# Kernel tuning notes

Hardware: AMD Instinct MI355X
Metric: run time of the kernel (lower is better)

The kernel has to match this reference:

```python
import jax, jax.numpy as jnp
import numpy as np

B, N, C, H = 8, 1024, 1024, 16
HD = C // H
SCALE = HD ** -0.5

def setup_inputs() -> dict:
    key = jax.random.key(0)
    k1, k2, k3, k4 = jax.random.split(key, 4)
    x = jax.random.normal(k1, (B, N, C), dtype=jnp.float32)
    # torch nn.Linear weights: [out, in]
    w_qkv = jax.random.normal(k2, (3 * C, C), dtype=jnp.float32) * (C ** -0.5)
    w_proj = jax.random.normal(k3, (C, C), dtype=jnp.float32) * (C ** -0.5)
    b_proj = jax.random.normal(k4, (C,), dtype=jnp.float32) * 0.02
    return {"x": x, "w_qkv": w_qkv, "w_proj": w_proj, "b_proj": b_proj}

def reference(x, w_qkv, w_proj, b_proj):
    Bv, Nv, Cv = x.shape
    # qkv projection (no bias); torch Linear: x @ W^T
    qkv = jnp.einsum('bnc,dc->bnd', x, w_qkv)
    qkv = qkv.reshape(Bv, Nv, 3, H, HD).transpose(2, 0, 3, 1, 4)  # [3,B,H,N,hd]
    q, k, v = qkv[0], qkv[1], qkv[2]
    attn = jnp.einsum('bhnd,bhmd->bhnm', q, k) * SCALE  # [B,H,N,N]
    attn = jax.nn.softmax(attn, axis=-1)
    out = jnp.einsum('bhnm,bhmd->bhnd', attn, v)
    out = out.transpose(0, 2, 1, 3).reshape(Bv, Nv, Cv)
    out = jnp.einsum('bnc,dc->bnd', out, w_proj) + b_proj
    return out
```

## Files before the change

kernel.cpp:

```cpp
#include <hip/hip_runtime.h>


typedef __attribute__((ext_vector_type(8))) short bf16x8;
typedef __attribute__((ext_vector_type(4))) float f32x4;

__device__ __forceinline__ short f2bf(float f) {
    union { float f; unsigned u; } x;
    x.f = f;
    unsigned r = x.u + 0x7fffu + ((x.u >> 16) & 1u);
    return (short)(r >> 16);
}

__device__ __forceinline__ void load_lds16(const void* g, void* l) {
    __builtin_amdgcn_global_load_lds((const __attribute__((address_space(1))) unsigned*)g,
                                     (__attribute__((address_space(3))) unsigned*)l,
                                     16, 0, 0);
}

__global__ __launch_bounds__(256) void convert_all(const float* __restrict__ x,
                                                   const float* __restrict__ wqkv,
                                                   const float* __restrict__ wproj,
                                                   short* __restrict__ xb,
                                                   short* __restrict__ wqkvb,
                                                   short* __restrict__ wprojb) {
    int i = blockIdx.x * 256 + threadIdx.x;
    const float* src;
    short* dst;
    int j;
    if (i < 2097152)      { src = x;     dst = xb;     j = i; }
    else if (i < 2883584) { src = wqkv;  dst = wqkvb;  j = i - 2097152; }
    else                  { src = wproj; dst = wprojb; j = i - 2883584; }
    float4 v = *(const float4*)(src + j * 4);
    unsigned lo = (unsigned short)f2bf(v.x) | ((unsigned)(unsigned short)f2bf(v.y) << 16);
    unsigned hi = (unsigned short)f2bf(v.z) | ((unsigned)(unsigned short)f2bf(v.w) << 16);
    uint2 p; p.x = lo; p.y = hi;
    *(uint2*)(dst + j * 4) = p;
}

__global__ __launch_bounds__(256) void gemm_qkv(const short* __restrict__ A,
                                                const short* __restrict__ Bt,
                                                short* __restrict__ q,
                                                short* __restrict__ k,
                                                short* __restrict__ vt) {
    __shared__ alignas(16) short As[3][128][32];
    __shared__ alignas(16) short Bs[3][128][32];
    const int K = 1024;
    const int m0 = blockIdx.y * 128;
    const int n0 = blockIdx.x * 128;
    const int t = threadIdx.x;
    const int w = t >> 6, lane = t & 63, quad = lane >> 4, l16 = lane & 15;
    const int wm = (w >> 1) * 64, wn = (w & 1) * 64;
    const int srow = lane >> 2;
    const int sc8 = (lane & 3) * 8;

    const short* Abase = &A[(m0 + w * 32 + srow) * K + sc8];
    const short* Bbase = &Bt[(n0 + w * 32 + srow) * K + sc8];

    f32x4 acc[4][4];
    for (int mi = 0; mi < 4; ++mi)
        for (int ni = 0; ni < 4; ++ni)
            acc[mi][ni] = (f32x4){0.f, 0.f, 0.f, 0.f};

    #pragma unroll
    for (int p = 0; p < 2; ++p) {
        load_lds16(Abase + p * 32,          &As[p][w * 32][0]);
        load_lds16(Abase + 16 * K + p * 32, &As[p][w * 32 + 16][0]);
        load_lds16(Bbase + p * 32,          &Bs[p][w * 32][0]);
        load_lds16(Bbase + 16 * K + p * 32, &Bs[p][w * 32 + 16][0]);
    }

    #pragma unroll
    for (int it = 0; it < 32; ++it) {
        if (it == 31) asm volatile("s_waitcnt vmcnt(0) lgkmcnt(0)" ::: "memory");
        else          asm volatile("s_waitcnt vmcnt(4) lgkmcnt(0)" ::: "memory");
        asm volatile("s_barrier" ::: "memory");
        if (it < 30) {
            const int b2 = (it + 2) % 3;
            load_lds16(Abase + (it + 2) * 32,          &As[b2][w * 32][0]);
            load_lds16(Abase + 16 * K + (it + 2) * 32, &As[b2][w * 32 + 16][0]);
            load_lds16(Bbase + (it + 2) * 32,          &Bs[b2][w * 32][0]);
            load_lds16(Bbase + 16 * K + (it + 2) * 32, &Bs[b2][w * 32 + 16][0]);
        }
        const int cb = it % 3;
        bf16x8 af[4], bfr[4];
        for (int i = 0; i < 4; ++i) af[i]  = *(const bf16x8*)&As[cb][wm + i * 16 + l16][quad * 8];
        for (int i = 0; i < 4; ++i) bfr[i] = *(const bf16x8*)&Bs[cb][wn + i * 16 + l16][quad * 8];
        for (int mi = 0; mi < 4; ++mi)
            for (int ni = 0; ni < 4; ++ni)
                acc[mi][ni] = __builtin_amdgcn_mfma_f32_16x16x32_bf16(af[mi], bfr[ni], acc[mi][ni], 0, 0, 0);
    }

    const float QS = 0.125f * 1.44269504088896f;
    for (int ni = 0; ni < 4; ++ni) {
        int col = n0 + wn + ni * 16 + l16;
        int sect = col >> 10;
        int c = col & 1023;
        int h = c >> 6, d = c & 63;
        for (int mi = 0; mi < 4; ++mi) {
            for (int r = 0; r < 4; ++r) {
                int m = m0 + wm + mi * 16 + quad * 4 + r;
                int b = m >> 10, i = m & 1023;
                float v = acc[mi][ni][r];
                if (sect == 0)      q[((b * 16 + h) * 1024 + i) * 64 + d] = f2bf(v * QS);
                else if (sect == 1) k[((b * 16 + h) * 1024 + i) * 64 + d] = f2bf(v);
                else                vt[((b * 16 + h) * 64 + d) * 1024 + i] = f2bf(v);
            }
        }
    }
}

__global__ __launch_bounds__(256) void attn_kernel(const short* __restrict__ q,
                                                   const short* __restrict__ k,
                                                   const short* __restrict__ vt,
                                                   short* __restrict__ ao) {
    __shared__ alignas(16) short Ks[64][72];
    __shared__ alignas(16) short Vs[64][72];
    __shared__ alignas(16) short Ps[4][32][72];

    const int bh = blockIdx.y, qt = blockIdx.x;
    const int t = threadIdx.x, w = t >> 6, lane = t & 63, quad = lane >> 4, l16 = lane & 15;
    const short* qg = q  + (bh * 1024 + qt * 128) * 64;
    const short* kg = k  + bh * 65536;
    const short* vg = vt + bh * 65536;

    bf16x8 qf[2][2];
    for (int mi = 0; mi < 2; ++mi) {
        const short* qr = qg + (w * 32 + mi * 16 + l16) * 64;
        qf[mi][0] = *(const bf16x8*)(qr + quad * 8);
        qf[mi][1] = *(const bf16x8*)(qr + 32 + quad * 8);
    }

    const int r0 = t >> 3,          c80 = (t & 7) * 8;
    const int r1 = (t + 256) >> 3,  c81 = c80;

    float rs[2][4];
    f32x4 oacc[2][4];
    for (int mi = 0; mi < 2; ++mi)
        for (int r = 0; r < 4; ++r) rs[mi][r] = 0.f;
    for (int mi = 0; mi < 2; ++mi)
        for (int nt = 0; nt < 4; ++nt) oacc[mi][nt] = (f32x4){0.f, 0.f, 0.f, 0.f};

    {
        float4 a = *(const float4*)&kg[r0 * 64 + c80];
        float4 b = *(const float4*)&kg[r1 * 64 + c81];
        float4 c = *(const float4*)&vg[r0 * 1024 + c80];
        float4 d = *(const float4*)&vg[r1 * 1024 + c81];
        *(float4*)&Ks[r0][c80] = a;  *(float4*)&Ks[r1][c81] = b;
        *(float4*)&Vs[r0][c80] = c;  *(float4*)&Vs[r1][c81] = d;
    }

    for (int jt = 0; jt < 16; ++jt) {
        asm volatile("s_waitcnt lgkmcnt(0)" ::: "memory");
        asm volatile("s_barrier" ::: "memory");

        float4 kr0, kr1, vr0, vr1;
        if (jt < 15) {
            int jn = jt + 1;
            kr0 = *(const float4*)&kg[(jn * 64 + r0) * 64 + c80];
            kr1 = *(const float4*)&kg[(jn * 64 + r1) * 64 + c81];
            vr0 = *(const float4*)&vg[r0 * 1024 + jn * 64 + c80];
            vr1 = *(const float4*)&vg[r1 * 1024 + jn * 64 + c81];
        }

        bf16x8 kf[4][2], vf[4][2];
        for (int nt = 0; nt < 4; ++nt) {
            kf[nt][0] = *(const bf16x8*)&Ks[nt * 16 + l16][quad * 8];
            kf[nt][1] = *(const bf16x8*)&Ks[nt * 16 + l16][32 + quad * 8];
            vf[nt][0] = *(const bf16x8*)&Vs[nt * 16 + l16][quad * 8];
            vf[nt][1] = *(const bf16x8*)&Vs[nt * 16 + l16][32 + quad * 8];
        }
        asm volatile("s_waitcnt lgkmcnt(0)" ::: "memory");
        asm volatile("s_barrier" ::: "memory");
        if (jt < 15) {
            *(float4*)&Ks[r0][c80] = kr0;  *(float4*)&Ks[r1][c81] = kr1;
            *(float4*)&Vs[r0][c80] = vr0;  *(float4*)&Vs[r1][c81] = vr1;
        }

        for (int mi = 0; mi < 2; ++mi) {
            f32x4 s[4];
            for (int nt = 0; nt < 4; ++nt) {
                f32x4 a = (f32x4){0.f, 0.f, 0.f, 0.f};
                a = __builtin_amdgcn_mfma_f32_16x16x32_bf16(qf[mi][0], kf[nt][0], a, 0, 0, 0);
                a = __builtin_amdgcn_mfma_f32_16x16x32_bf16(qf[mi][1], kf[nt][1], a, 0, 0, 0);
                s[nt] = a;
            }
            for (int nt = 0; nt < 4; ++nt) {
                for (int r = 0; r < 4; ++r) {
                    float p = __builtin_amdgcn_exp2f(s[nt][r]);
                    rs[mi][r] += p;
                    Ps[w][mi * 16 + quad * 4 + r][nt * 16 + l16] = f2bf(p);
                }
            }
            asm volatile("s_waitcnt lgkmcnt(0)" ::: "memory");
            bf16x8 pa0 = *(const bf16x8*)&Ps[w][mi * 16 + l16][quad * 8];
            bf16x8 pa1 = *(const bf16x8*)&Ps[w][mi * 16 + l16][32 + quad * 8];
            for (int nt = 0; nt < 4; ++nt) {
                oacc[mi][nt] = __builtin_amdgcn_mfma_f32_16x16x32_bf16(pa0, vf[nt][0], oacc[mi][nt], 0, 0, 0);
                oacc[mi][nt] = __builtin_amdgcn_mfma_f32_16x16x32_bf16(pa1, vf[nt][1], oacc[mi][nt], 0, 0, 0);
            }
        }
    }

    for (int mi = 0; mi < 2; ++mi)
        for (int r = 0; r < 4; ++r)
            for (int msk = 1; msk < 16; msk <<= 1)
                rs[mi][r] += __shfl_xor(rs[mi][r], msk, 64);

    const int b = bh >> 4, h = bh & 15;
    for (int mi = 0; mi < 2; ++mi) {
        for (int r = 0; r < 4; ++r) {
            float inv = 1.0f / rs[mi][r];
            int i = qt * 128 + w * 32 + mi * 16 + quad * 4 + r;
            for (int nt = 0; nt < 4; ++nt) {
                int d = nt * 16 + l16;
                ao[(b * 1024 + i) * 1024 + h * 64 + d] = f2bf(oacc[mi][nt][r] * inv);
            }
        }
    }
}

__global__ __launch_bounds__(256) void gemm_proj(const short* __restrict__ A,
                                                 const short* __restrict__ Bt,
                                                 const float* __restrict__ bias,
                                                 float* __restrict__ out) {
    __shared__ alignas(16) short As[3][128][32];
    __shared__ alignas(16) short Bs[3][128][32];
    const int K = 1024;
    const int m0 = blockIdx.y * 128;
    const int n0 = blockIdx.x * 128;
    const int t = threadIdx.x;
    const int w = t >> 6, lane = t & 63, quad = lane >> 4, l16 = lane & 15;
    const int wm = (w >> 1) * 64, wn = (w & 1) * 64;
    const int srow = lane >> 2;
    const int sc8 = (lane & 3) * 8;

    const short* Abase = &A[(m0 + w * 32 + srow) * K + sc8];
    const short* Bbase = &Bt[(n0 + w * 32 + srow) * K + sc8];

    f32x4 acc[4][4];
    for (int mi = 0; mi < 4; ++mi)
        for (int ni = 0; ni < 4; ++ni)
            acc[mi][ni] = (f32x4){0.f, 0.f, 0.f, 0.f};

    #pragma unroll
    for (int p = 0; p < 2; ++p) {
        load_lds16(Abase + p * 32,          &As[p][w * 32][0]);
        load_lds16(Abase + 16 * K + p * 32, &As[p][w * 32 + 16][0]);
        load_lds16(Bbase + p * 32,          &Bs[p][w * 32][0]);
        load_lds16(Bbase + 16 * K + p * 32, &Bs[p][w * 32 + 16][0]);
    }

    #pragma unroll
    for (int it = 0; it < 32; ++it) {
        if (it == 31) asm volatile("s_waitcnt vmcnt(0) lgkmcnt(0)" ::: "memory");
        else          asm volatile("s_waitcnt vmcnt(4) lgkmcnt(0)" ::: "memory");
        asm volatile("s_barrier" ::: "memory");
        if (it < 30) {
            const int b2 = (it + 2) % 3;
            load_lds16(Abase + (it + 2) * 32,          &As[b2][w * 32][0]);
            load_lds16(Abase + 16 * K + (it + 2) * 32, &As[b2][w * 32 + 16][0]);
            load_lds16(Bbase + (it + 2) * 32,          &Bs[b2][w * 32][0]);
            load_lds16(Bbase + 16 * K + (it + 2) * 32, &Bs[b2][w * 32 + 16][0]);
        }
        const int cb = it % 3;
        bf16x8 af[4], bfr[4];
        for (int i = 0; i < 4; ++i) af[i]  = *(const bf16x8*)&As[cb][wm + i * 16 + l16][quad * 8];
        for (int i = 0; i < 4; ++i) bfr[i] = *(const bf16x8*)&Bs[cb][wn + i * 16 + l16][quad * 8];
        for (int mi = 0; mi < 4; ++mi)
            for (int ni = 0; ni < 4; ++ni)
                acc[mi][ni] = __builtin_amdgcn_mfma_f32_16x16x32_bf16(af[mi], bfr[ni], acc[mi][ni], 0, 0, 0);
    }

    for (int ni = 0; ni < 4; ++ni) {
        int col = n0 + wn + ni * 16 + l16;
        float bv = bias[col];
        for (int mi = 0; mi < 4; ++mi) {
            for (int r = 0; r < 4; ++r) {
                int m = m0 + wm + mi * 16 + quad * 4 + r;
                out[m * 1024 + col] = acc[mi][ni][r] + bv;
            }
        }
    }
}

extern "C" void kernel_launch(void* const* d_in, const int* in_sizes, int n_in,
                              void* d_out, int out_size, void* d_ws, size_t ws_size,
                              hipStream_t stream) {
    const float* x      = (const float*)d_in[0];
    const float* w_qkv  = (const float*)d_in[1];
    const float* w_proj = (const float*)d_in[2];
    const float* b_proj = (const float*)d_in[3];
    float* out = (float*)d_out;

    char* ws = (char*)d_ws;
    short* xb     = (short*)(ws);
    short* wqkvb  = (short*)(ws + 16777216);
    short* wprojb = (short*)(ws + 23068672);
    short* qb     = (short*)(ws + 25165824);
    short* kb     = (short*)(ws + 41943040);
    short* vtb    = (short*)(ws + 58720256);
    short* aob    = (short*)(ws + 75497472);

    convert_all<<<12288, 256, 0, stream>>>(x, w_qkv, w_proj, xb, wqkvb, wprojb);
    gemm_qkv<<<dim3(24, 64), 256, 0, stream>>>(xb, wqkvb, qb, kb, vtb);
    attn_kernel<<<dim3(8, 128), 256, 0, stream>>>(qb, kb, vtb, aob);
    gemm_proj<<<dim3(8, 64), 256, 0, stream>>>(aob, wprojb, b_proj, out);
}
```

Measured before the change: 280.3 us.

## Compute transposed S so P stays in registers, dropping the LDS round-trip

The attention kernel now computes S^T = K·Q^T, so each lane's MFMA output already matches the B-operand layout of a 16x16x16 bf16 MFMA. P therefore feeds the PV product straight from registers, and the per-warp P shared buffer with its writes, waits and reads is removed. The output is accumulated transposed (O^T = V^T·P^T), which makes the row-sum reduction shorter and lets the final store write 4 bf16 at a time. In exchange it uses twice as many smaller 16x16x16 MFMAs for PV and reads V from LDS in narrower 8-byte fragments.

```diff
diff --git a/kernel.cpp b/kernel.cpp
--- a/kernel.cpp
+++ b/kernel.cpp
@@ -2,6 +2,7 @@
 
 
 typedef __attribute__((ext_vector_type(8))) short bf16x8;
+typedef __attribute__((ext_vector_type(4))) short bf16x4;
 typedef __attribute__((ext_vector_type(4))) float f32x4;
 
 __device__ __forceinline__ short f2bf(float f) {
@@ -115,7 +116,6 @@
                                                    short* __restrict__ ao) {
     __shared__ alignas(16) short Ks[64][72];
     __shared__ alignas(16) short Vs[64][72];
-    __shared__ alignas(16) short Ps[4][32][72];
 
     const int bh = blockIdx.y, qt = blockIdx.x;
     const int t = threadIdx.x, w = t >> 6, lane = t & 63, quad = lane >> 4, l16 = lane & 15;
@@ -133,12 +133,10 @@
     const int r0 = t >> 3,          c80 = (t & 7) * 8;
     const int r1 = (t + 256) >> 3,  c81 = c80;
 
-    float rs[2][4];
-    f32x4 oacc[2][4];
+    float rs[2] = {0.f, 0.f};
+    f32x4 oaccT[2][4];
     for (int mi = 0; mi < 2; ++mi)
-        for (int r = 0; r < 4; ++r) rs[mi][r] = 0.f;
-    for (int mi = 0; mi < 2; ++mi)
-        for (int nt = 0; nt < 4; ++nt) oacc[mi][nt] = (f32x4){0.f, 0.f, 0.f, 0.f};
+        for (int dt = 0; dt < 4; ++dt) oaccT[mi][dt] = (f32x4){0.f, 0.f, 0.f, 0.f};
 
     {
         float4 a = *(const float4*)&kg[r0 * 64 + c80];
@@ -162,12 +160,13 @@
             vr1 = *(const float4*)&vg[r1 * 1024 + jn * 64 + c81];
         }
 
-        bf16x8 kf[4][2], vf[4][2];
-        for (int nt = 0; nt < 4; ++nt) {
-            kf[nt][0] = *(const bf16x8*)&Ks[nt * 16 + l16][quad * 8];
-            kf[nt][1] = *(const bf16x8*)&Ks[nt * 16 + l16][32 + quad * 8];
-            vf[nt][0] = *(const bf16x8*)&Vs[nt * 16 + l16][quad * 8];
-            vf[nt][1] = *(const bf16x8*)&Vs[nt * 16 + l16][32 + quad * 8];
+        bf16x8 kf[4][2];
+        bf16x4 vtf[4][4];
+        for (int js = 0; js < 4; ++js) {
+            kf[js][0] = *(const bf16x8*)&Ks[js * 16 + l16][quad * 8];
+            kf[js][1] = *(const bf16x8*)&Ks[js * 16 + l16][32 + quad * 8];
+            for (int dt = 0; dt < 4; ++dt)
+                vtf[js][dt] = *(const bf16x4*)&Vs[dt * 16 + l16][js * 16 + quad * 4];
         }
         asm volatile("s_waitcnt lgkmcnt(0)" ::: "memory");
         asm volatile("s_barrier" ::: "memory");
@@ -177,44 +176,37 @@
         }
 
         for (int mi = 0; mi < 2; ++mi) {
-            f32x4 s[4];
-            for (int nt = 0; nt < 4; ++nt) {
-                f32x4 a = (f32x4){0.f, 0.f, 0.f, 0.f};
-                a = __builtin_amdgcn_mfma_f32_16x16x32_bf16(qf[mi][0], kf[nt][0], a, 0, 0, 0);
-                a = __builtin_amdgcn_mfma_f32_16x16x32_bf16(qf[mi][1], kf[nt][1], a, 0, 0, 0);
-                s[nt] = a;
+            for (int js = 0; js < 4; ++js) {
+                f32x4 s = (f32x4){0.f, 0.f, 0.f, 0.f};
+                s = __builtin_amdgcn_mfma_f32_16x16x32_bf16(kf[js][0], qf[mi][0], s, 0, 0, 0);
+                s = __builtin_amdgcn_mfma_f32_16x16x32_bf16(kf[js][1], qf[mi][1], s, 0, 0, 0);
+                bf16x4 pfrag;
+                for (int r = 0; r < 4; ++r) {
+                    float p = __builtin_amdgcn_exp2f(s[r]);
+                    rs[mi] += p;
+                    pfrag[r] = f2bf(p);
+                }
+                for (int dt = 0; dt < 4; ++dt)
+                    oaccT[mi][dt] = __builtin_amdgcn_mfma_f32_16x16x16bf16_1k(
+                        vtf[js][dt], pfrag, oaccT[mi][dt], 0, 0, 0);
             }
-            for (int nt = 0; nt < 4; ++nt) {
-                for (int r = 0; r < 4; ++r) {
-                    float p = __builtin_amdgcn_exp2f(s[nt][r]);
-                    rs[mi][r] += p;
-                    Ps[w][mi * 16 + quad * 4 + r][nt * 16 + l16] = f2bf(p);
-                }
-            }
-            asm volatile("s_waitcnt lgkmcnt(0)" ::: "memory");
-            bf16x8 pa0 = *(const bf16x8*)&Ps[w][mi * 16 + l16][quad * 8];
-            bf16x8 pa1 = *(const bf16x8*)&Ps[w][mi * 16 + l16][32 + quad * 8];
-            for (int nt = 0; nt < 4; ++nt) {
-                oacc[mi][nt] = __builtin_amdgcn_mfma_f32_16x16x32_bf16(pa0, vf[nt][0], oacc[mi][nt], 0, 0, 0);
-                oacc[mi][nt] = __builtin_amdgcn_mfma_f32_16x16x32_bf16(pa1, vf[nt][1], oacc[mi][nt], 0, 0, 0);
-            }
-        }
-    }
-
-    for (int mi = 0; mi < 2; ++mi)
-        for (int r = 0; r < 4; ++r)
-            for (int msk = 1; msk < 16; msk <<= 1)
-                rs[mi][r] += __shfl_xor(rs[mi][r], msk, 64);
+        }
+    }
+
+    for (int mi = 0; mi < 2; ++mi) {
+        rs[mi] += __shfl_xor(rs[mi], 16, 64);
+        rs[mi] += __shfl_xor(rs[mi], 32, 64);
+    }
 
     const int b = bh >> 4, h = bh & 15;
     for (int mi = 0; mi < 2; ++mi) {
-        for (int r = 0; r < 4; ++r) {
-            float inv = 1.0f / rs[mi][r];
-            int i = qt * 128 + w * 32 + mi * 16 + quad * 4 + r;
-            for (int nt = 0; nt < 4; ++nt) {
-                int d = nt * 16 + l16;
-                ao[(b * 1024 + i) * 1024 + h * 64 + d] = f2bf(oacc[mi][nt][r] * inv);
-            }
+        float inv = 1.0f / rs[mi];
+        int i = qt * 128 + w * 32 + mi * 16 + l16;
+        short* aor = ao + (b * 1024 + i) * 1024 + h * 64;
+        for (int dt = 0; dt < 4; ++dt) {
+            bf16x4 o4;
+            for (int r = 0; r < 4; ++r) o4[r] = f2bf(oaccT[mi][dt][r] * inv);
+            *(bf16x4*)(aor + dt * 16 + quad * 4) = o4;
         }
     }
 }
```

After: 267.0 us. 4.8% less time.
